# Optimization experiments

Measured on AMD Instinct MI355X. Metric: run time of the kernel, lower is better.

Reference implementation:

```python
import jax, jax.numpy as jnp
import numpy as np

B, A, C, D = 64, 1024, 64, 512
NEG = -9.0e15


def _ln(x, w, b, eps=1e-5):
    mu = jnp.mean(x, axis=-1, keepdims=True)
    var = jnp.mean((x - mu) ** 2, axis=-1, keepdims=True)
    return (x - mu) * jax.lax.rsqrt(var + eps) * w + b


def setup_inputs() -> dict:
    key = jax.random.key(0)
    ks = jax.random.split(key, 8)
    att_index = np.arange(A) % C
    am = np.zeros((C, A), np.float32)
    am[att_index, np.arange(A)] = 1.0 / (A // C)  # avgmask[i,j]=1/count if att_index[j]==i
    adj_ha = np.concatenate([am, np.eye(C, dtype=np.float32)], axis=1)      # [C, A+C]
    adj_ah = np.concatenate([am.T, np.eye(A, dtype=np.float32)], axis=1)    # [A, C+A]
    w = lambda k: jax.random.normal(k, (D, D), jnp.float32) * 0.05
    ones, zeros = jnp.ones((D,), jnp.float32), jnp.zeros((D,), jnp.float32)
    return {
        "att_vf": jax.random.normal(ks[0], (B, A, D), jnp.float32) * 0.05,
        "avgmask": jnp.asarray(am), "adj_ha": jnp.asarray(adj_ha), "adj_ah": jnp.asarray(adj_ah),
        "l1_W_h2h": w(ks[1]), "l1_W_h2a": w(ks[2]),
        "l1_ln1_w": ones, "l1_ln1_b": zeros, "l1_ln2_w": ones, "l1_ln2_b": zeros,
        "l1_ln3_w": ones, "l1_ln3_b": zeros,
        "l2_W_a2h": w(ks[3]), "l2_W_h2h": w(ks[4]), "l2_W_h2a": w(ks[5]),
        "l2_ln1_w": ones, "l2_ln1_b": zeros, "l2_ln2_w": ones, "l2_ln2_b": zeros,
        "l2_ln3_w": ones, "l2_ln3_b": zeros,
    }


def _forward(att_vf, avgmask, adj_ha, adj_ah,
             l1_W_h2h, l1_W_h2a, l1_ln1_w, l1_ln1_b, l1_ln2_w, l1_ln2_b, l1_ln3_w, l1_ln3_b,
             l2_W_a2h, l2_W_h2h, l2_W_h2a, l2_ln1_w, l2_ln1_b, l2_ln2_w, l2_ln2_b, l2_ln3_w, l2_ln3_b):
    inv_sd = 1.0 / jnp.sqrt(jnp.float32(D))  # input_dim == h_dim == D

    def h2h(hl, W, lw, lb):
        hln = _ln(hl, lw, lb)                                  # [B,C,D]
        hide = hln @ W
        s = jnp.einsum('bid,bjd->bij', hide, hide) * inv_sd
        a = jax.nn.softmax(s, axis=-1)
        return jnp.einsum('bij,bjd->bid', a, hln)

    def h2a(upd_hl, att, W, lw, lb):
        hln = _ln(upd_hl, lw, lb)
        hidden = jnp.concatenate([hln @ W, att], axis=1)       # [B, C+A, D]
        s = jnp.einsum('bad,bkd->bak', att, hidden) * inv_sd   # [B, A, C+A]
        s = jnp.where(adj_ah > 0, s, NEG)
        a = jax.nn.softmax(s, axis=-1)
        return jnp.einsum('bak,bkd->bad', a, hidden)

    # layer 1: a2h = 'avg'
    hl = jnp.einsum('ca,bad->bcd', avgmask, _ln(att_vf, l1_ln1_w, l1_ln1_b))  # [B,C,D]
    hl1 = h2h(hl, l1_W_h2h, l1_ln2_w, l1_ln2_b)
    att1 = h2a(hl1, att_vf, l1_W_h2a, l1_ln3_w, l1_ln3_b)

    # layer 2: a2h = 'attention'
    att_ln = _ln(att1, l2_ln1_w, l2_ln1_b)
    hidden = jnp.concatenate([att_ln @ l2_W_a2h, hl1], axis=1)  # [B, A+C, D]
    s = jnp.einsum('bcd,bkd->bck', hl1, hidden) * inv_sd        # [B, C, A+C]
    s = jnp.where(adj_ha > 0, s, NEG)
    hl2 = jnp.einsum('bck,bkd->bcd', jax.nn.softmax(s, axis=-1), hidden)
    hl2 = h2h(hl2, l2_W_h2h, l2_ln2_w, l2_ln2_b)
    att2 = h2a(hl2, att1, l2_W_h2a, l2_ln3_w, l2_ln3_b)
    return att2


def reference(att_vf, avgmask, adj_ha, adj_ah,
              l1_W_h2h, l1_W_h2a, l1_ln1_w, l1_ln1_b, l1_ln2_w, l1_ln2_b, l1_ln3_w, l1_ln3_b,
              l2_W_a2h, l2_W_h2h, l2_W_h2a, l2_ln1_w, l2_ln1_b, l2_ln2_w, l2_ln2_b, l2_ln3_w, l2_ln3_b):
    return _forward(att_vf, avgmask, adj_ha, adj_ah,
                    l1_W_h2h, l1_W_h2a, l1_ln1_w, l1_ln1_b, l1_ln2_w, l1_ln2_b, l1_ln3_w, l1_ln3_b,
                    l2_W_a2h, l2_W_h2h, l2_W_h2a, l2_ln1_w, l2_ln1_b, l2_ln2_w, l2_ln2_b, l2_ln3_w, l2_ln3_b)
```

## Files before the change

kernel.cpp:

```cpp
#include <hip/hip_runtime.h>

#define B_ 64
#define A_ 1024
#define C_ 64
#define D_ 512
#define INV_SD 0.044194173824159216f

typedef __bf16 bf16_t;
typedef __bf16 bf16x8 __attribute__((ext_vector_type(8)));
typedef __bf16 bf16x2 __attribute__((ext_vector_type(2)));
typedef float f32x4 __attribute__((ext_vector_type(4)));

static __device__ __forceinline__ bf16_t f2b(float x) { return (bf16_t)x; }
static __device__ __forceinline__ float b2f(bf16_t x) { return (float)x; }

static __device__ __forceinline__ void gl_lds16(const void* g, void* l) {
  __builtin_amdgcn_global_load_lds(
      (const __attribute__((address_space(1))) unsigned int*)g,
      (__attribute__((address_space(3))) unsigned int*)l, 16, 0, 0);
}

__global__ __launch_bounds__(256) void k_hl0(const float* __restrict__ att,
                                             const float* __restrict__ lw1,
                                             const float* __restrict__ lb1,
                                             const float* __restrict__ lw2,
                                             const float* __restrict__ lb2,
                                             bf16_t* __restrict__ hlnb) {
  int blk = blockIdx.x;
  int b = blk >> 6, c = blk & 63;
  int t = threadIdx.x;
  int w = t >> 6, lane = t & 63;
  __shared__ float part[4][512];
  __shared__ float reds[8];
  float ps[8] = {0.f, 0.f, 0.f, 0.f, 0.f, 0.f, 0.f, 0.f};
#pragma unroll
  for (int i = 0; i < 4; ++i) {
    int jj = w * 4 + i;
    const float* xr = att + ((size_t)b * A_ + jj * 64 + c) * D_ + lane * 8;
    float4 v1 = *(const float4*)xr;
    float4 v2 = *(const float4*)(xr + 4);
    float v[8] = {v1.x, v1.y, v1.z, v1.w, v2.x, v2.y, v2.z, v2.w};
    float s = 0.f, q = 0.f;
#pragma unroll
    for (int u = 0; u < 8; ++u) { s += v[u]; q += v[u] * v[u]; }
#pragma unroll
    for (int o = 32; o; o >>= 1) { s += __shfl_xor(s, o); q += __shfl_xor(q, o); }
    float mu = s * (1.0f / D_);
    float rs = rsqrtf(q * (1.0f / D_) - mu * mu + 1e-5f);
#pragma unroll
    for (int u = 0; u < 8; ++u) ps[u] += (v[u] - mu) * rs;
  }
#pragma unroll
  for (int u = 0; u < 8; ++u) part[w][lane * 8 + u] = ps[u];
  __syncthreads();
  int d = 2 * t;
  float hx = ((part[0][d] + part[1][d]) + (part[2][d] + part[3][d])) * (1.f / 16.f) * lw1[d] + lb1[d];
  float hy = ((part[0][d + 1] + part[1][d + 1]) + (part[2][d + 1] + part[3][d + 1])) * (1.f / 16.f) * lw1[d + 1] + lb1[d + 1];
  float s = hx + hy, q = hx * hx + hy * hy;
#pragma unroll
  for (int o = 32; o; o >>= 1) { s += __shfl_xor(s, o); q += __shfl_xor(q, o); }
  if (lane == 0) { reds[w] = s; reds[4 + w] = q; }
  __syncthreads();
  float S = (reds[0] + reds[1]) + (reds[2] + reds[3]);
  float Q = (reds[4] + reds[5]) + (reds[6] + reds[7]);
  float mu = S * (1.0f / D_);
  float rs = rsqrtf(Q * (1.0f / D_) - mu * mu + 1e-5f);
  bf16x2 ob;
  ob.x = f2b((hx - mu) * rs * lw2[d] + lb2[d]);
  ob.y = f2b((hy - mu) * rs * lw2[d + 1] + lb2[d + 1]);
  *(bf16x2*)(hlnb + (size_t)blk * D_ + d) = ob;
}

__global__ __launch_bounds__(256) void k_lnb_bf(const bf16_t* __restrict__ x,
                                                const float* __restrict__ lw,
                                                const float* __restrict__ lb,
                                                bf16_t* __restrict__ yb) {
  int t = threadIdx.x;
  int row = blockIdx.x * 4 + (t >> 6);
  int lane = t & 63;
  int d0 = lane * 8;
  bf16x8 xb = *(const bf16x8*)(x + (size_t)row * D_ + d0);
  float v[8];
#pragma unroll
  for (int u = 0; u < 8; ++u) v[u] = b2f(xb[u]);
  float s = 0.f, q = 0.f;
#pragma unroll
  for (int u = 0; u < 8; ++u) { s += v[u]; q += v[u] * v[u]; }
#pragma unroll
  for (int o = 32; o; o >>= 1) { s += __shfl_xor(s, o); q += __shfl_xor(q, o); }
  float mu = s * (1.0f / D_);
  float rs = rsqrtf(q * (1.0f / D_) - mu * mu + 1e-5f);
  float4 w1 = *(const float4*)(lw + d0);
  float4 w2 = *(const float4*)(lw + d0 + 4);
  float4 b1 = *(const float4*)(lb + d0);
  float4 b2 = *(const float4*)(lb + d0 + 4);
  float lwv[8] = {w1.x, w1.y, w1.z, w1.w, w2.x, w2.y, w2.z, w2.w};
  float lbv[8] = {b1.x, b1.y, b1.z, b1.w, b2.x, b2.y, b2.z, b2.w};
  bf16x8 ob;
#pragma unroll
  for (int u = 0; u < 8; ++u) ob[u] = f2b((v[u] - mu) * rs * lwv[u] + lbv[u]);
  *(bf16x8*)(yb + (size_t)row * D_ + d0) = ob;
}

__global__ __launch_bounds__(256) void k_tr(const bf16_t* __restrict__ src,
                                            bf16_t* __restrict__ dst) {
  __shared__ unsigned short sm[64][72];
  int n0 = blockIdx.x;
  int b = blockIdx.y;
  int t = threadIdx.x;
  const bf16_t* sb = src + (size_t)b * C_ * D_;
  bf16_t* db = dst + (size_t)b * D_ * C_;
#pragma unroll
  for (int rep = 0; rep < 2; ++rep) {
    int f = t + rep * 256;
    int r = f >> 3, c8 = f & 7;
    uint4 v = *(const uint4*)(sb + (size_t)r * D_ + n0 * 64 + c8 * 8);
    unsigned int* p = (unsigned int*)&sm[r][c8 * 8];
    p[0] = v.x; p[1] = v.y; p[2] = v.z; p[3] = v.w;
  }
  __syncthreads();
#pragma unroll
  for (int rep = 0; rep < 2; ++rep) {
    int f = t + rep * 256;
    int nr = f >> 3, c8 = f & 7;
    unsigned short tmp[8];
#pragma unroll
    for (int u = 0; u < 8; ++u) tmp[u] = sm[c8 * 8 + u][nr];
    *(uint4*)(db + (size_t)(n0 * 64 + nr) * 64 + c8 * 8) = *(const uint4*)tmp;
  }
}

__global__ __launch_bounds__(256) void k_wt6(const float* __restrict__ W0, const float* __restrict__ W1,
                                             const float* __restrict__ W2, const float* __restrict__ W3,
                                             const float* __restrict__ W4, bf16_t* __restrict__ WtBase) {
  __shared__ float tile[64][65];
  const float* Ws[5] = {W0, W1, W2, W3, W4};
  int z = blockIdx.z;
  int k0 = blockIdx.x * 64;
  int n0 = blockIdx.y * 64;
  int t = threadIdx.x;
  int r0 = t >> 6;
  int c = t & 63;
  if (z == 5) {
    const float* W = Ws[2];
    bf16_t* Wt = WtBase + (size_t)5 * 512 * 512;
#pragma unroll 4
    for (int i = 0; i < 16; ++i) {
      int r = r0 * 16 + i;
      Wt[(size_t)(k0 + r) * 512 + n0 + c] = f2b(W[(size_t)(k0 + r) * 512 + n0 + c]);
    }
    return;
  }
  const float* W = Ws[z];
  bf16_t* Wt = WtBase + (size_t)z * 512 * 512;
#pragma unroll 4
  for (int i = 0; i < 16; ++i) {
    int r = r0 * 16 + i;
    tile[r][c] = W[(size_t)(k0 + r) * 512 + n0 + c];
  }
  __syncthreads();
#pragma unroll 4
  for (int i = 0; i < 16; ++i) {
    int r = r0 * 16 + i;
    Wt[(size_t)(n0 + r) * 512 + k0 + c] = f2b(tile[c][r]);
  }
}

template <int BM, bool BIAS>
__global__ __launch_bounds__(256, 4) void k_mfma_gemm(const bf16_t* __restrict__ Abf,
                                                      const bf16_t* __restrict__ Wt,
                                                      const bf16_t* __restrict__ Rb,
                                                      bf16_t* __restrict__ Cmat) {
  constexpr int TR = BM / 32;
  constexpr int ABYTES = BM * 128;
  constexpr int CBYTES = BM * 136 * 2;
  constexpr int SMEM = (ABYTES + 16384 > CBYTES) ? (ABYTES + 16384) : CBYTES;
  __shared__ char smem[SMEM];
  bf16_t* As = (bf16_t*)smem;
  bf16_t* Bs = (bf16_t*)(smem + ABYTES);

  int t = threadIdx.x;
  int lane = t & 63, wave = t >> 6;
  int wr = wave >> 1, wc = wave & 1;
  int lhi = lane >> 4, llo = lane & 15;

  int nwg = gridDim.x;
  int bid = blockIdx.x;
  int tile = (bid & 7) * (nwg >> 3) + (bid >> 3);
  int bm = tile >> 2, bn = tile & 3;

  const bf16_t* Ab = Abf + (size_t)bm * BM * 512;
  const bf16_t* Wb = Wt + (size_t)bn * 128 * 512;

  int l3 = lane >> 3;
  int srcOff = ((lane & 7) ^ l3) * 8;

  auto stage = [&](int k0) {
#pragma unroll
    for (int i = 0; i < BM / 32; ++i) {
      int r0 = wave * (BM / 4) + i * 8;
      gl_lds16(Ab + (size_t)(r0 + l3) * 512 + k0 + srcOff, As + r0 * 64);
    }
#pragma unroll
    for (int i = 0; i < 4; ++i) {
      int r0 = wave * 32 + i * 8;
      gl_lds16(Wb + (size_t)(r0 + l3) * 512 + k0 + srcOff, Bs + r0 * 64);
    }
  };

  f32x4 acc[TR][4] = {};
  stage(0);
  __syncthreads();

  for (int k0 = 0; k0 < 512; k0 += 64) {
#pragma unroll
    for (int kk = 0; kk < 2; ++kk) {
      bf16x8 af[TR], bfr[4];
      int bofs = kk * 64 + lhi * 16;
#pragma unroll
      for (int tr = 0; tr < TR; ++tr) {
        int row = wr * (BM / 2) + tr * 16 + llo;
        af[tr] = *(const bf16x8*)((const char*)As + row * 128 + (bofs ^ ((row & 7) << 4)));
      }
#pragma unroll
      for (int tc = 0; tc < 4; ++tc) {
        int col = wc * 64 + tc * 16 + llo;
        bfr[tc] = *(const bf16x8*)((const char*)Bs + col * 128 + (bofs ^ ((col & 7) << 4)));
      }
#pragma unroll
      for (int tr = 0; tr < TR; ++tr)
#pragma unroll
        for (int tc = 0; tc < 4; ++tc)
          acc[tr][tc] = __builtin_amdgcn_mfma_f32_16x16x32_bf16(af[tr], bfr[tc], acc[tr][tc], 0, 0, 0);
    }
    if (k0 + 64 < 512) {
      __syncthreads();
      stage(k0 + 64);
      __syncthreads();
    }
  }

  __syncthreads();
  bf16_t(*Cs)[136] = (bf16_t(*)[136])smem;
#pragma unroll
  for (int tr = 0; tr < TR; ++tr) {
    int row = wr * (BM / 2) + tr * 16 + lhi * 4;
#pragma unroll
    for (int r = 0; r < 4; ++r)
#pragma unroll
      for (int tc = 0; tc < 4; ++tc) {
        float v = acc[tr][tc][r];
        if constexpr (BIAS)
          v += b2f(Rb[(size_t)(bm * BM + row + r) * 512 + bn * 128 + wc * 64 + tc * 16 + llo]);
        Cs[row + r][wc * 64 + tc * 16 + llo] = f2b(v);
      }
  }
  __syncthreads();
#pragma unroll
  for (int i = 0; i < BM / 16; ++i) {
    int row = i * 16 + wave * 4 + lhi;
    uint4 v = *(const uint4*)(&Cs[row][llo * 8]);
    *(uint4*)(Cmat + (size_t)(bm * BM + row) * 512 + bn * 128 + llo * 8) = v;
  }
}

template <int MODE>
__global__ __launch_bounds__(256) void k_h2h(const bf16_t* __restrict__ hide,
                                             const bf16_t* __restrict__ hlnT,
                                             const float* __restrict__ lnw,
                                             const float* __restrict__ lnbv,
                                             float* __restrict__ hl1f,
                                             bf16_t* __restrict__ hl1b,
                                             bf16_t* __restrict__ lnout) {
  __shared__ bf16_t hS[8 * 64 * 64];
  __shared__ float sS[16][68];
  __shared__ bf16_t wS[16 * 64];
  __shared__ float mur[16], rsr[16];

  int q = blockIdx.x;
  int b = blockIdx.y;
  int t = threadIdx.x;
  int lane = t & 63, wave = t >> 6;
  int lhi = lane >> 4, llo = lane & 15;

  const bf16_t* Hb = hide + (size_t)b * C_ * D_;
#pragma unroll
  for (int rep = 0; rep < 16; ++rep) {
    int f = t + rep * 256;
    int row = f >> 6, c16 = f & 63;
    int kc = c16 >> 3, ci = c16 & 7;
    uint4 v = *(const uint4*)(Hb + (size_t)row * 512 + c16 * 8);
    *(uint4*)((char*)hS + kc * 8192 + row * 128 + ((ci * 16) ^ ((row & 7) << 4))) = v;
  }
  __syncthreads();

  {
    f32x4 acc = {};
#pragma unroll
    for (int ks = 0; ks < 16; ++ks) {
      int kc = ks >> 1;
      int bofs = (ks & 1) * 64 + lhi * 16;
      int ra = q * 16 + llo;
      int rb = wave * 16 + llo;
      bf16x8 af = *(const bf16x8*)((const char*)hS + kc * 8192 + ra * 128 + (bofs ^ ((ra & 7) << 4)));
      bf16x8 bf = *(const bf16x8*)((const char*)hS + kc * 8192 + rb * 128 + (bofs ^ ((rb & 7) << 4)));
      acc = __builtin_amdgcn_mfma_f32_16x16x32_bf16(af, bf, acc, 0, 0, 0);
    }
#pragma unroll
    for (int r = 0; r < 4; ++r) sS[lhi * 4 + r][wave * 16 + llo] = acc[r] * INV_SD;
  }
  __syncthreads();

  if (t < 128) {
    int row = t >> 3, sg = t & 7;
    float v[8];
#pragma unroll
    for (int u = 0; u < 8; ++u) v[u] = sS[row][sg * 8 + u];
    float m = v[0];
#pragma unroll
    for (int u = 1; u < 8; ++u) m = fmaxf(m, v[u]);
#pragma unroll
    for (int o = 4; o; o >>= 1) m = fmaxf(m, __shfl_xor(m, o));
    float sum = 0.f;
#pragma unroll
    for (int u = 0; u < 8; ++u) { v[u] = __expf(v[u] - m); sum += v[u]; }
#pragma unroll
    for (int o = 4; o; o >>= 1) sum += __shfl_xor(sum, o);
    float inv = 1.f / sum;
    bf16x8 wv;
#pragma unroll
    for (int u = 0; u < 8; ++u) wv[u] = f2b(v[u] * inv);
    *(bf16x8*)((char*)wS + row * 128 + ((sg * 16) ^ ((row & 7) << 4))) = wv;
  }
  __syncthreads();

  float* sf = (float*)hS;
  {
    bf16x8 af[2];
#pragma unroll
    for (int ks = 0; ks < 2; ++ks)
      af[ks] = *(const bf16x8*)((const char*)wS + llo * 128 + (((ks * 64 + lhi * 16)) ^ ((llo & 7) << 4)));
    const bf16_t* Tb = hlnT + (size_t)b * D_ * C_;
#pragma unroll
    for (int nt = 0; nt < 8; ++nt) {
      int dcol = wave * 128 + nt * 16 + llo;
      f32x4 acc = {};
#pragma unroll
      for (int ks = 0; ks < 2; ++ks) {
        bf16x8 bf = *(const bf16x8*)(Tb + (size_t)dcol * 64 + ks * 32 + lhi * 8);
        acc = __builtin_amdgcn_mfma_f32_16x16x32_bf16(af[ks], bf, acc, 0, 0, 0);
      }
#pragma unroll
      for (int r = 0; r < 4; ++r) sf[(lhi * 4 + r) * 516 + dcol] = acc[r];
    }
  }
  __syncthreads();

  {
    int lr = t >> 4, p = t & 15;
    float s = 0.f, q2 = 0.f;
#pragma unroll 8
    for (int i = 0; i < 32; ++i) {
      float v = sf[lr * 516 + p + 16 * i];
      s += v;
      q2 += v * v;
    }
#pragma unroll
    for (int o = 8; o; o >>= 1) { s += __shfl_xor(s, o); q2 += __shfl_xor(q2, o); }
    if (p == 0) {
      float mu = s * (1.0f / D_);
      mur[lr] = mu;
      rsr[lr] = rsqrtf(q2 * (1.0f / D_) - mu * mu + 1e-5f);
    }
  }
  __syncthreads();

  int d = 2 * t;
  float lwx = lnw[d], lwy = lnw[d + 1], lbx = lnbv[d], lby = lnbv[d + 1];
#pragma unroll 4
  for (int r = 0; r < 16; ++r) {
    float2 xy = *(const float2*)(&sf[r * 516 + d]);
    size_t go = ((size_t)b * C_ + q * 16 + r) * 512 + d;
    float mu = mur[r], rs = rsr[r];
    if constexpr (MODE == 0) {
      *(float2*)(hl1f + go) = xy;
      bf16x2 hb;
      hb.x = f2b(xy.x);
      hb.y = f2b(xy.y);
      *(bf16x2*)(hl1b + go) = hb;
    }
    bf16x2 lb2;
    lb2.x = f2b((xy.x - mu) * rs * lwx + lbx);
    lb2.y = f2b((xy.y - mu) * rs * lwy + lby);
    *(bf16x2*)(lnout + go) = lb2;
  }
}

__global__ __launch_bounds__(256) void k_h2a_ln(const float* __restrict__ att,
                                                const bf16_t* __restrict__ hW,
                                                bf16_t* __restrict__ att1b,
                                                float* __restrict__ stats) {
  int t = threadIdx.x;
  int row = blockIdx.x * 4 + (t >> 6);
  int lane = t & 63;
  int b = row >> 10, a = row & 1023;
  int c = a & 63;
  int d0 = lane * 8;
  const float* ar = att + (size_t)row * D_ + d0;
  const bf16_t* wr = hW + (size_t)(b * 64 + c) * D_ + d0;
  float4 a1 = *(const float4*)ar;
  float4 a2 = *(const float4*)(ar + 4);
  bf16x8 wb = *(const bf16x8*)wr;
  float w[8], av[8] = {a1.x, a1.y, a1.z, a1.w, a2.x, a2.y, a2.z, a2.w};
#pragma unroll
  for (int u = 0; u < 8; ++u) w[u] = b2f(wb[u]);
  float d1 = 0.f, d2 = 0.f;
#pragma unroll
  for (int u = 0; u < 8; ++u) { d1 += av[u] * w[u]; d2 += av[u] * av[u]; }
#pragma unroll
  for (int o = 32; o; o >>= 1) { d1 += __shfl_xor(d1, o); d2 += __shfl_xor(d2, o); }
  float s1 = d1 * INV_SD, s2 = d2 * INV_SD;
  float m = fmaxf(s1, s2);
  float e1 = __expf(s1 - m), e2 = __expf(s2 - m);
  float inv = 1.f / (e1 + e2);
  float alpha = e1 * inv, beta = e2 * inv;
  float o8[8];
  float s = 0.f, q = 0.f;
#pragma unroll
  for (int u = 0; u < 8; ++u) {
    o8[u] = alpha * w[u] + beta * av[u];
    s += o8[u];
    q += o8[u] * o8[u];
  }
  bf16x8 ob;
#pragma unroll
  for (int u = 0; u < 8; ++u) ob[u] = f2b(o8[u]);
  *(bf16x8*)(att1b + (size_t)row * D_ + d0) = ob;
#pragma unroll
  for (int o = 32; o; o >>= 1) { s += __shfl_xor(s, o); q += __shfl_xor(q, o); }
  if (lane == 0) {
    float mu = s * (1.0f / D_);
    stats[2 * row] = mu;
    stats[2 * row + 1] = rsqrtf(q * (1.0f / D_) - mu * mu + 1e-5f);
  }
}

__global__ __launch_bounds__(256) void k_h2a_out(const bf16_t* __restrict__ att,
                                                 const bf16_t* __restrict__ hW,
                                                 float* __restrict__ outp) {
  int t = threadIdx.x;
  int row = blockIdx.x * 4 + (t >> 6);
  int lane = t & 63;
  int b = row >> 10, a = row & 1023;
  int c = a & 63;
  int d0 = lane * 8;
  bf16x8 ab = *(const bf16x8*)(att + (size_t)row * D_ + d0);
  bf16x8 wb = *(const bf16x8*)(hW + (size_t)(b * 64 + c) * D_ + d0);
  float av[8], w[8];
#pragma unroll
  for (int u = 0; u < 8; ++u) { av[u] = b2f(ab[u]); w[u] = b2f(wb[u]); }
  float d1 = 0.f, d2 = 0.f;
#pragma unroll
  for (int u = 0; u < 8; ++u) { d1 += av[u] * w[u]; d2 += av[u] * av[u]; }
#pragma unroll
  for (int o = 32; o; o >>= 1) { d1 += __shfl_xor(d1, o); d2 += __shfl_xor(d2, o); }
  float s1 = d1 * INV_SD, s2 = d2 * INV_SD;
  float m = fmaxf(s1, s2);
  float e1 = __expf(s1 - m), e2 = __expf(s2 - m);
  float inv = 1.f / (e1 + e2);
  float alpha = e1 * inv, beta = e2 * inv;
  float4 o1, o2;
  o1.x = alpha * w[0] + beta * av[0]; o1.y = alpha * w[1] + beta * av[1];
  o1.z = alpha * w[2] + beta * av[2]; o1.w = alpha * w[3] + beta * av[3];
  o2.x = alpha * w[4] + beta * av[4]; o2.y = alpha * w[5] + beta * av[5];
  o2.z = alpha * w[6] + beta * av[6]; o2.w = alpha * w[7] + beta * av[7];
  float* orow = outp + (size_t)row * D_ + d0;
  *(float4*)orow = o1;
  *(float4*)(orow + 4) = o2;
}

__global__ __launch_bounds__(256) void k_a2h_u(const float* __restrict__ hl1f,
                                               const bf16_t* __restrict__ G,
                                               const bf16_t* __restrict__ att1b,
                                               const float* __restrict__ stats,
                                               const float* __restrict__ lw,
                                               const float* __restrict__ lb,
                                               bf16_t* __restrict__ u_out,
                                               bf16_t* __restrict__ R_out) {
  int blk = blockIdx.x;
  int b = blk >> 6, c = blk & 63;
  int t = threadIdx.x;
  int wave = t >> 6, lane = t & 63;
  __shared__ float hrow[512], grow[512], lwS[512], lbS[512];
  __shared__ bf16_t lnS[16][512];
  __shared__ float wts[32];
  __shared__ float red[4];
  {
    int d = 2 * t;
    float2 h2 = *(const float2*)(hl1f + (size_t)blk * 512 + d);
    hrow[d] = h2.x;
    hrow[d + 1] = h2.y;
    bf16x2 g2 = *(const bf16x2*)(G + (size_t)blk * 512 + d);
    grow[d] = b2f(g2.x);
    grow[d + 1] = b2f(g2.y);
    float2 w2 = *(const float2*)(lw + d);
    lwS[d] = w2.x;
    lwS[d + 1] = w2.y;
    float2 bb = *(const float2*)(lb + d);
    lbS[d] = bb.x;
    lbS[d + 1] = bb.y;
    float sd = h2.x * h2.x + h2.y * h2.y;
#pragma unroll
    for (int o = 32; o; o >>= 1) sd += __shfl_xor(sd, o);
    if (lane == 0) red[wave] = sd;
  }
  __syncthreads();
#pragma unroll
  for (int i = 0; i < 4; ++i) {
    int j = wave * 4 + i;
    size_t row = (size_t)b * A_ + j * 64 + c;
    float mu = stats[2 * row], rs = stats[2 * row + 1];
    bf16x8 x = *(const bf16x8*)(att1b + row * 512 + lane * 8);
    float dot = 0.f;
    bf16x8 lnv;
#pragma unroll
    for (int u = 0; u < 8; ++u) {
      int k = lane * 8 + u;
      float v = (b2f(x[u]) - mu) * rs * lwS[k] + lbS[k];
      lnv[u] = f2b(v);
      dot += v * grow[k];
    }
    *(bf16x8*)(&lnS[j][lane * 8]) = lnv;
#pragma unroll
    for (int o = 32; o; o >>= 1) dot += __shfl_xor(dot, o);
    if (lane == 0) wts[j] = dot * INV_SD;
  }
  if (t == 0) wts[16] = ((red[0] + red[1]) + (red[2] + red[3])) * INV_SD;
  __syncthreads();
  if (t < 64) {
    float val = (t < 17) ? wts[t] : -3.0e38f;
    float m = val;
#pragma unroll
    for (int o = 32; o; o >>= 1) m = fmaxf(m, __shfl_xor(m, o));
    float e = (t < 17) ? __expf(val - m) : 0.f;
    float ssum = e;
#pragma unroll
    for (int o = 32; o; o >>= 1) ssum += __shfl_xor(ssum, o);
    if (t < 17) wts[t] = e / ssum;
  }
  __syncthreads();
  int d = 2 * t;
  float ux = 0.f, uy = 0.f;
#pragma unroll 4
  for (int jj = 0; jj < 16; ++jj) {
    bf16x2 l2 = *(const bf16x2*)(&lnS[jj][d]);
    ux += wts[jj] * b2f(l2.x);
    uy += wts[jj] * b2f(l2.y);
  }
  bf16x2 uo, ro;
  uo.x = f2b(ux);
  uo.y = f2b(uy);
  *(bf16x2*)(u_out + (size_t)blk * 512 + d) = uo;
  float w16 = wts[16];
  ro.x = f2b(w16 * hrow[d]);
  ro.y = f2b(w16 * hrow[d + 1]);
  *(bf16x2*)(R_out + (size_t)blk * 512 + d) = ro;
}

extern "C" void kernel_launch(void* const* d_in, const int* in_sizes, int n_in,
                              void* d_out, int out_size, void* d_ws, size_t ws_size,
                              hipStream_t stream) {
  const float* att_vf = (const float*)d_in[0];
  const float* W1_h2h = (const float*)d_in[4];
  const float* W1_h2a = (const float*)d_in[5];
  const float* ln11w = (const float*)d_in[6];
  const float* ln11b = (const float*)d_in[7];
  const float* ln12w = (const float*)d_in[8];
  const float* ln12b = (const float*)d_in[9];
  const float* ln13w = (const float*)d_in[10];
  const float* ln13b = (const float*)d_in[11];
  const float* W2_a2h = (const float*)d_in[12];
  const float* W2_h2h = (const float*)d_in[13];
  const float* W2_h2a = (const float*)d_in[14];
  const float* ln21w = (const float*)d_in[15];
  const float* ln21b = (const float*)d_in[16];
  const float* ln22w = (const float*)d_in[17];
  const float* ln22b = (const float*)d_in[18];
  const float* ln23w = (const float*)d_in[19];
  const float* ln23b = (const float*)d_in[20];
  float* out = (float*)d_out;

  float* ws = (float*)d_ws;
  const size_t SM = (size_t)B_ * C_ * D_;
  float* hl1f = ws;
  bf16_t* A1b = (bf16_t*)(hl1f + SM);
  bf16_t* A1t = (bf16_t*)((float*)A1b + SM / 2);
  bf16_t* A2b = (bf16_t*)((float*)A1t + SM / 2);
  bf16_t* hl1b = (bf16_t*)((float*)A2b + SM / 2);
  bf16_t* u_b = (bf16_t*)((float*)hl1b + SM / 2);
  bf16_t* R_b = (bf16_t*)((float*)u_b + SM / 2);
  bf16_t* Wt0 = (bf16_t*)((float*)R_b + SM / 2);
  const size_t WTE = (size_t)512 * 512;
  bf16_t* att1b = Wt0 + 6 * WTE;
  float* stats = (float*)(att1b + (size_t)B_ * A_ * D_);

  dim3 blk(256);
  k_wt6<<<dim3(8, 8, 6), blk, 0, stream>>>(W1_h2h, W1_h2a, W2_a2h, W2_h2h, W2_h2a, Wt0);

  k_hl0<<<B_ * C_, blk, 0, stream>>>(att_vf, ln11w, ln11b, ln12w, ln12b, A1b);
  k_tr<<<dim3(8, B_), blk, 0, stream>>>(A1b, A1t);
  k_mfma_gemm<64, false><<<256, blk, 0, stream>>>(A1b, Wt0 + 0 * WTE, nullptr, A2b);
  k_h2h<0><<<dim3(4, B_), blk, 0, stream>>>(A2b, A1t, ln13w, ln13b, hl1f, hl1b, A1b);
  k_mfma_gemm<64, false><<<256, blk, 0, stream>>>(A1b, Wt0 + 1 * WTE, nullptr, A2b);
  k_h2a_ln<<<(B_ * A_) / 4, blk, 0, stream>>>(att_vf, A2b, att1b, stats);
  k_mfma_gemm<64, false><<<256, blk, 0, stream>>>(hl1b, Wt0 + 5 * WTE, nullptr, A2b);
  k_a2h_u<<<B_ * C_, blk, 0, stream>>>(hl1f, A2b, att1b, stats, ln21w, ln21b, u_b, R_b);
  k_mfma_gemm<64, true><<<256, blk, 0, stream>>>(u_b, Wt0 + 2 * WTE, R_b, A2b);
  k_lnb_bf<<<(B_ * C_) / 4, blk, 0, stream>>>(A2b, ln22w, ln22b, A1b);
  k_tr<<<dim3(8, B_), blk, 0, stream>>>(A1b, A1t);
  k_mfma_gemm<64, false><<<256, blk, 0, stream>>>(A1b, Wt0 + 3 * WTE, nullptr, A2b);
  k_h2h<1><<<dim3(4, B_), blk, 0, stream>>>(A2b, A1t, ln23w, ln23b, nullptr, nullptr, A1b);
  k_mfma_gemm<64, false><<<256, blk, 0, stream>>>(A1b, Wt0 + 4 * WTE, nullptr, A2b);
  k_h2a_out<<<(B_ * A_) / 4, blk, 0, stream>>>(att1b, A2b, out);
}
```

Measured before the change: 208.5 us.

## Double-buffer GEMM LDS staging and fuse LayerNorm with transpose

The MFMA GEMM now uses two LDS buffers, prefetching the next K tile while computing the current one, with a single barrier per iteration instead of two. The launch bound occupancy hint drops to fit the doubled shared memory. Separately, the layer-2 LayerNorm and the following transpose are merged into one kernel per batch that writes both row-major and transposed outputs through LDS, removing a launch and a global round trip. The fused kernel uses only 64 blocks, which limits parallelism.

```diff
diff --git a/kernel.cpp b/kernel.cpp
--- a/kernel.cpp
+++ b/kernel.cpp
@@ -71,35 +71,52 @@
   *(bf16x2*)(hlnb + (size_t)blk * D_ + d) = ob;
 }
 
-__global__ __launch_bounds__(256) void k_lnb_bf(const bf16_t* __restrict__ x,
-                                                const float* __restrict__ lw,
-                                                const float* __restrict__ lb,
-                                                bf16_t* __restrict__ yb) {
-  int t = threadIdx.x;
-  int row = blockIdx.x * 4 + (t >> 6);
-  int lane = t & 63;
+__global__ __launch_bounds__(256) void k_ln_tr(const bf16_t* __restrict__ x,
+                                               const float* __restrict__ lw,
+                                               const float* __restrict__ lb,
+                                               bf16_t* __restrict__ y,
+                                               bf16_t* __restrict__ yt) {
+  __shared__ bf16_t lnS[64][528];
+  int b = blockIdx.x;
+  int t = threadIdx.x;
+  int wv = t >> 6, lane = t & 63;
   int d0 = lane * 8;
-  bf16x8 xb = *(const bf16x8*)(x + (size_t)row * D_ + d0);
-  float v[8];
-#pragma unroll
-  for (int u = 0; u < 8; ++u) v[u] = b2f(xb[u]);
-  float s = 0.f, q = 0.f;
-#pragma unroll
-  for (int u = 0; u < 8; ++u) { s += v[u]; q += v[u] * v[u]; }
-#pragma unroll
-  for (int o = 32; o; o >>= 1) { s += __shfl_xor(s, o); q += __shfl_xor(q, o); }
-  float mu = s * (1.0f / D_);
-  float rs = rsqrtf(q * (1.0f / D_) - mu * mu + 1e-5f);
   float4 w1 = *(const float4*)(lw + d0);
   float4 w2 = *(const float4*)(lw + d0 + 4);
   float4 b1 = *(const float4*)(lb + d0);
   float4 b2 = *(const float4*)(lb + d0 + 4);
   float lwv[8] = {w1.x, w1.y, w1.z, w1.w, w2.x, w2.y, w2.z, w2.w};
   float lbv[8] = {b1.x, b1.y, b1.z, b1.w, b2.x, b2.y, b2.z, b2.w};
-  bf16x8 ob;
-#pragma unroll
-  for (int u = 0; u < 8; ++u) ob[u] = f2b((v[u] - mu) * rs * lwv[u] + lbv[u]);
-  *(bf16x8*)(yb + (size_t)row * D_ + d0) = ob;
+  const bf16_t* xb = x + (size_t)b * C_ * D_;
+  bf16_t* yb = y + (size_t)b * C_ * D_;
+#pragma unroll 4
+  for (int i = 0; i < 16; ++i) {
+    int r = wv * 16 + i;
+    bf16x8 xv = *(const bf16x8*)(xb + (size_t)r * D_ + d0);
+    float v[8], s = 0.f, q = 0.f;
+#pragma unroll
+    for (int u = 0; u < 8; ++u) { v[u] = b2f(xv[u]); s += v[u]; q += v[u] * v[u]; }
+#pragma unroll
+    for (int o = 32; o; o >>= 1) { s += __shfl_xor(s, o); q += __shfl_xor(q, o); }
+    float mu = s * (1.0f / D_);
+    float rs = rsqrtf(q * (1.0f / D_) - mu * mu + 1e-5f);
+    bf16x8 ob;
+#pragma unroll
+    for (int u = 0; u < 8; ++u) ob[u] = f2b((v[u] - mu) * rs * lwv[u] + lbv[u]);
+    *(bf16x8*)(yb + (size_t)r * D_ + d0) = ob;
+    *(bf16x8*)(&lnS[r][d0]) = ob;
+  }
+  __syncthreads();
+  bf16_t* tb = yt + (size_t)b * D_ * C_;
+#pragma unroll
+  for (int pass = 0; pass < 16; ++pass) {
+    int d = pass * 32 + (t >> 3);
+    int c0 = (t & 7) * 8;
+    unsigned short tmp[8];
+#pragma unroll
+    for (int u = 0; u < 8; ++u) tmp[u] = *(const unsigned short*)&lnS[c0 + u][d];
+    *(uint4*)(tb + (size_t)d * 64 + c0) = *(const uint4*)tmp;
+  }
 }
 
 __global__ __launch_bounds__(256) void k_tr(const bf16_t* __restrict__ src,
@@ -167,17 +184,15 @@
 }
 
 template <int BM, bool BIAS>
-__global__ __launch_bounds__(256, 4) void k_mfma_gemm(const bf16_t* __restrict__ Abf,
+__global__ __launch_bounds__(256, 3) void k_mfma_gemm(const bf16_t* __restrict__ Abf,
                                                       const bf16_t* __restrict__ Wt,
                                                       const bf16_t* __restrict__ Rb,
                                                       bf16_t* __restrict__ Cmat) {
   constexpr int TR = BM / 32;
   constexpr int ABYTES = BM * 128;
-  constexpr int CBYTES = BM * 136 * 2;
-  constexpr int SMEM = (ABYTES + 16384 > CBYTES) ? (ABYTES + 16384) : CBYTES;
-  __shared__ char smem[SMEM];
-  bf16_t* As = (bf16_t*)smem;
-  bf16_t* Bs = (bf16_t*)(smem + ABYTES);
+  constexpr int BBYTES = 128 * 128;
+  constexpr int BUF = ABYTES + BBYTES;
+  __shared__ char smem[2 * BUF];
 
   int t = threadIdx.x;
   int lane = t & 63, wave = t >> 6;
@@ -195,24 +210,30 @@
   int l3 = lane >> 3;
   int srcOff = ((lane & 7) ^ l3) * 8;
 
-  auto stage = [&](int k0) {
+  auto stage = [&](int k0, int bi) {
+    char* As = smem + bi * BUF;
+    char* Bs = As + ABYTES;
 #pragma unroll
     for (int i = 0; i < BM / 32; ++i) {
       int r0 = wave * (BM / 4) + i * 8;
-      gl_lds16(Ab + (size_t)(r0 + l3) * 512 + k0 + srcOff, As + r0 * 64);
+      gl_lds16(Ab + (size_t)(r0 + l3) * 512 + k0 + srcOff, As + r0 * 128);
     }
 #pragma unroll
     for (int i = 0; i < 4; ++i) {
       int r0 = wave * 32 + i * 8;
-      gl_lds16(Wb + (size_t)(r0 + l3) * 512 + k0 + srcOff, Bs + r0 * 64);
+      gl_lds16(Wb + (size_t)(r0 + l3) * 512 + k0 + srcOff, Bs + r0 * 128);
     }
   };
 
   f32x4 acc[TR][4] = {};
-  stage(0);
-  __syncthreads();
-
-  for (int k0 = 0; k0 < 512; k0 += 64) {
+  stage(0, 0);
+  __syncthreads();
+
+  for (int it = 0; it < 8; ++it) {
+    int cur = it & 1;
+    if (it < 7) stage((it + 1) * 64, cur ^ 1);
+    const char* As = smem + cur * BUF;
+    const char* Bs = As + ABYTES;
 #pragma unroll
     for (int kk = 0; kk < 2; ++kk) {
       bf16x8 af[TR], bfr[4];
@@ -220,12 +241,12 @@
 #pragma unroll
       for (int tr = 0; tr < TR; ++tr) {
         int row = wr * (BM / 2) + tr * 16 + llo;
-        af[tr] = *(const bf16x8*)((const char*)As + row * 128 + (bofs ^ ((row & 7) << 4)));
+        af[tr] = *(const bf16x8*)(As + row * 128 + (bofs ^ ((row & 7) << 4)));
       }
 #pragma unroll
       for (int tc = 0; tc < 4; ++tc) {
         int col = wc * 64 + tc * 16 + llo;
-        bfr[tc] = *(const bf16x8*)((const char*)Bs + col * 128 + (bofs ^ ((col & 7) << 4)));
+        bfr[tc] = *(const bf16x8*)(Bs + col * 128 + (bofs ^ ((col & 7) << 4)));
       }
 #pragma unroll
       for (int tr = 0; tr < TR; ++tr)
@@ -233,14 +254,9 @@
         for (int tc = 0; tc < 4; ++tc)
           acc[tr][tc] = __builtin_amdgcn_mfma_f32_16x16x32_bf16(af[tr], bfr[tc], acc[tr][tc], 0, 0, 0);
     }
-    if (k0 + 64 < 512) {
-      __syncthreads();
-      stage(k0 + 64);
-      __syncthreads();
-    }
-  }
-
-  __syncthreads();
+    __syncthreads();
+  }
+
   bf16_t(*Cs)[136] = (bf16_t(*)[136])smem;
 #pragma unroll
   for (int tr = 0; tr < TR; ++tr) {
@@ -616,8 +632,7 @@
   k_mfma_gemm<64, false><<<256, blk, 0, stream>>>(hl1b, Wt0 + 5 * WTE, nullptr, A2b);
   k_a2h_u<<<B_ * C_, blk, 0, stream>>>(hl1f, A2b, att1b, stats, ln21w, ln21b, u_b, R_b);
   k_mfma_gemm<64, true><<<256, blk, 0, stream>>>(u_b, Wt0 + 2 * WTE, R_b, A2b);
-  k_lnb_bf<<<(B_ * C_) / 4, blk, 0, stream>>>(A2b, ln22w, ln22b, A1b);
-  k_tr<<<dim3(8, B_), blk, 0, stream>>>(A1b, A1t);
+  k_ln_tr<<<B_, blk, 0, stream>>>(A2b, ln22w, ln22b, A1b, A1t);
   k_mfma_gemm<64, false><<<256, blk, 0, stream>>>(A1b, Wt0 + 3 * WTE, nullptr, A2b);
   k_h2h<1><<<dim3(4, B_), blk, 0, stream>>>(A2b, A1t, ln23w, ln23b, nullptr, nullptr, A1b);
   k_mfma_gemm<64, false><<<256, blk, 0, stream>>>(A1b, Wt0 + 4 * WTE, nullptr, A2b);
```

Measured after the change: 207.6 us. Within noise of the previous version (-0.5%).
